# Performance work log

Measured on AMD Instinct MI355X. Metric: run time of the kernel, lower is better.

The kernel has to match this reference:

```python
import jax, jax.numpy as jnp
import numpy as np

D_MODEL = 1024
NUM_HEADS = 16
D_K = D_MODEL // NUM_HEADS


def setup_inputs() -> dict:
    key = jax.random.key(0)
    ks = jax.random.split(key, 11)
    B, S = 1, 4096
    s = 1.0 / np.sqrt(D_MODEL)
    return {
        "query": jax.random.normal(ks[0], (B, S, D_MODEL), jnp.float32),
        "key": jax.random.normal(ks[1], (B, S, D_MODEL), jnp.float32),
        "value": jax.random.normal(ks[2], (B, S, D_MODEL), jnp.float32),
        "Wq": jax.random.normal(ks[3], (D_MODEL, D_MODEL), jnp.float32) * s,
        "bq": jnp.zeros((D_MODEL,), jnp.float32),
        "Wk": jax.random.normal(ks[4], (D_MODEL, D_MODEL), jnp.float32) * s,
        "bk": jnp.zeros((D_MODEL,), jnp.float32),
        "Wv": jax.random.normal(ks[5], (D_MODEL, D_MODEL), jnp.float32) * s,
        "bv": jnp.zeros((D_MODEL,), jnp.float32),
        "Wo": jax.random.normal(ks[6], (D_MODEL, D_MODEL), jnp.float32) * s,
        "bo": jnp.zeros((D_MODEL,), jnp.float32),
    }


def reference(query, key, value, Wq, bq, Wk, bk, Wv, bv, Wo, bo):
    B, S, _ = query.shape
    # linear projections, split into heads: [B, H, S, d_k]
    def proj(x, W, b):
        y = x @ W.T + b
        return y.reshape(B, -1, NUM_HEADS, D_K).transpose(0, 2, 1, 3)

    q = proj(query, Wq, bq)
    k = proj(key, Wk, bk)
    v = proj(value, Wv, bv)

    scale = D_K ** (-0.5)
    scores = jnp.einsum("bhqd,bhkd->bhqk", q, k) * scale  # [B,H,S,S]
    attn = jax.nn.softmax(scores, axis=-1)
    out = jnp.einsum("bhqk,bhkd->bhqd", attn, v)  # [B,H,S,d_k]
    out = out.transpose(0, 2, 1, 3).reshape(B, -1, NUM_HEADS * D_K)
    return out @ Wo.T + bo
```

## Files before the change

### kernel.cpp

```cpp
#include <hip/hip_runtime.h>

typedef __bf16 bf16;
typedef __bf16 bf16x8 __attribute__((ext_vector_type(8)));
typedef __bf16 bf16x4 __attribute__((ext_vector_type(4)));
typedef float floatx4 __attribute__((ext_vector_type(4)));

#define MFMA(a, b, c) __builtin_amdgcn_mfma_f32_16x16x32_bf16((a), (b), (c), 0, 0, 0)

__device__ inline bf16x8 load8(const bf16* p) { return *(const bf16x8*)(p); }
__device__ inline bf16x4 load4(const bf16* p) { return *(const bf16x4*)(p); }
__device__ inline bf16x8 cat44(bf16x4 a, bf16x4 b) {
    return __builtin_shufflevector(a, b, 0, 1, 2, 3, 4, 5, 6, 7);
}

__device__ inline void store_c(bf16* p, float v) { *p = (bf16)v; }
__device__ inline void store_c(float* p, float v) { *p = v; }

__device__ inline float fast_exp2(float x) {
#if __has_builtin(__builtin_amdgcn_exp2f)
    return __builtin_amdgcn_exp2f(x);
#else
    float r;
    asm("v_exp_f32 %0, %1" : "=v"(r) : "v"(x));
    return r;
#endif
}

__device__ inline float fast_rcp(float x) {
#if __has_builtin(__builtin_amdgcn_rcpf)
    return __builtin_amdgcn_rcpf(x);
#else
    float r;
    asm("v_rcp_f32 %0, %1" : "=v"(r) : "v"(x));
    return r;
#endif
}

__device__ inline void gload_lds(const bf16* g, bf16* l) {
    __builtin_amdgcn_global_load_lds(
        (const __attribute__((address_space(1))) void*)(g),
        (__attribute__((address_space(3))) void*)(l), 16, 0, 0);
}

struct CvtArgs {
    const float* src[7];
    bf16* dst[7];
    int n[7];
};
__global__ __launch_bounds__(256) void cvt_bf16(CvtArgs a) {
    const int t = blockIdx.y;
    const int i = (blockIdx.x * 256 + threadIdx.x) * 8;
    if (i >= a.n[t]) return;
    const float4 u = *(const float4*)(a.src[t] + i);
    const float4 v = *(const float4*)(a.src[t] + i + 4);
    bf16x8 r;
    r[0] = (bf16)u.x; r[1] = (bf16)u.y; r[2] = (bf16)u.z; r[3] = (bf16)u.w;
    r[4] = (bf16)v.x; r[5] = (bf16)v.y; r[6] = (bf16)v.z; r[7] = (bf16)v.w;
    *(bf16x8*)(a.dst[t] + i) = r;
}

template <typename TC>
__device__ inline void gemm_core(const bf16* __restrict__ A, const bf16* __restrict__ W,
                                 const float* __restrict__ bias, TC* __restrict__ C,
                                 bool TR) {
    __shared__ bf16 As[2][128][32];
    __shared__ bf16 Bs[2][128][32];

    const int tid = threadIdx.x;
    const int wv = tid >> 6, lane = tid & 63;
    const int quad = lane >> 4, lo = lane & 15;
    const int wm = wv >> 1, wn = wv & 1;
    const int Ar0 = blockIdx.y * 128, Br0 = blockIdx.x * 128;

    const int srow = lane >> 2, sseg = (lane & 3) ^ (srow & 3);
    const bf16* Ag = A + (size_t)(Ar0 + srow) * 1024 + sseg * 8;
    const bf16* Bg = W + (size_t)(Br0 + srow) * 1024 + sseg * 8;

    auto stage = [&](int buf, int k0) {
#pragma unroll
        for (int c = 2 * wv; c < 2 * wv + 2; c++) {
            gload_lds(Ag + (size_t)c * 16 * 1024 + k0, &As[buf][c * 16][0]);
            gload_lds(Bg + (size_t)c * 16 * 1024 + k0, &Bs[buf][c * 16][0]);
        }
    };

    floatx4 acc[4][4] = {};
    const int rs = (quad ^ (lo & 3)) * 8;

    stage(0, 0);
    for (int k0 = 0; k0 < 1024; k0 += 32) {
        const int buf = (k0 >> 5) & 1;
        __syncthreads();
        if (k0 + 32 < 1024) stage(buf ^ 1, k0 + 32);

        bf16x8 a[4], b[4];
#pragma unroll
        for (int i = 0; i < 4; i++) a[i] = load8(&As[buf][wm * 64 + i * 16 + lo][rs]);
#pragma unroll
        for (int j = 0; j < 4; j++) b[j] = load8(&Bs[buf][wn * 64 + j * 16 + lo][rs]);
#pragma unroll
        for (int i = 0; i < 4; i++)
#pragma unroll
            for (int j = 0; j < 4; j++) acc[i][j] = MFMA(a[i], b[j], acc[i][j]);
    }

#pragma unroll
    for (int i = 0; i < 4; i++) {
#pragma unroll
        for (int j = 0; j < 4; j++) {
#pragma unroll
            for (int r = 0; r < 4; r++) {
                const int m = Ar0 + wm * 64 + i * 16 + quad * 4 + r;
                const int n = Br0 + wn * 64 + j * 16 + lo;
                const float v = acc[i][j][r] + bias[n];
                if (!TR) {
                    store_c(C + (size_t)m * 1024 + n, v);
                } else {
                    store_c(C + (size_t)(n >> 6) * (64 * 4096) + (size_t)(n & 63) * 4096 + m, v);
                }
            }
        }
    }
}

__global__ __launch_bounds__(256) void gemm_qkv(
    const bf16* __restrict__ qb, const bf16* __restrict__ kb, const bf16* __restrict__ vb,
    const bf16* __restrict__ Wq, const bf16* __restrict__ Wk, const bf16* __restrict__ Wv,
    const float* __restrict__ bq, const float* __restrict__ bk, const float* __restrict__ bv,
    bf16* __restrict__ Q, bf16* __restrict__ Kp, bf16* __restrict__ Vt) {
    if (blockIdx.z == 0)
        gemm_core<bf16>(qb, Wq, bq, Q, false);
    else if (blockIdx.z == 1)
        gemm_core<bf16>(kb, Wk, bk, Kp, false);
    else
        gemm_core<bf16>(vb, Wv, bv, Vt, true);
}

__global__ __launch_bounds__(256) void gemm_o(const bf16* __restrict__ O,
                                              const bf16* __restrict__ Wo,
                                              const float* __restrict__ bo,
                                              float* __restrict__ out) {
    gemm_core<float>(O, Wo, bo, out, false);
}

__global__ __launch_bounds__(512) void flash_attn14(const bf16* __restrict__ Q,
                                                    const bf16* __restrict__ Kmat,
                                                    const bf16* __restrict__ Vt,
                                                    float* __restrict__ Pp,
                                                    float* __restrict__ lb) {
    __shared__ bf16 Ks[4][64][64];
    __shared__ bf16 Vs[4][64][64];

    const int tid = threadIdx.x;
    const int wv = tid >> 6;
    const int lane = tid & 63;
    const int quad = lane >> 4, lo = lane & 15;
    const int h = blockIdx.x;
    const int qb = blockIdx.y;
    const int z = blockIdx.z;
    const int kv0 = z * 2048;
    const int DM = 1024;
    const int q0 = qb * 256 + wv * 32;

    float* myP = Pp + (size_t)z * 4096 * 1024;
    float* myl = lb + z * 65536 + h * 4096;

    bf16x8 aQ[2][2];
#pragma unroll
    for (int qs = 0; qs < 2; qs++) {
        const bf16* qp = Q + (size_t)(q0 + qs * 16 + lo) * DM + h * 64 + quad * 8;
        aQ[qs][0] = load8(qp);
        aQ[qs][1] = load8(qp + 32);
    }

    bf16x8 bOnes;
#pragma unroll
    for (int i = 0; i < 8; i++) bOnes[i] = (bf16)1.0f;

    floatx4 Oacc[2][4] = {};
    floatx4 Lacc[2] = {};

    const int srow = lane >> 3, sseg = (lane & 7) ^ srow;
    const bf16* Kg = Kmat + (size_t)srow * DM + h * 64 + sseg * 8;
    const bf16* Vg = Vt + (size_t)h * 64 * 4096 + (size_t)srow * 4096 + sseg * 8;

    auto stage = [&](int buf, int kb2) {
        gload_lds(Kg + (size_t)(kb2 + wv * 8) * DM, &Ks[buf][wv * 8][0]);
        gload_lds(Vg + (size_t)(wv * 8) * 4096 + kb2, &Vs[buf][wv * 8][0]);
    };

    const float C_SCALE = 0.18033688011112043f;
    const float C_BIAS = 23.083120654223415f;
    const int sw = lo & 7;
    const int vo = quad >> 1;
    const int vlo = (quad & 1) * 4;

    auto body = [&](int buf) {
        floatx4 st[2][4];
        __builtin_amdgcn_s_setprio(1);
#pragma unroll
        for (int t = 0; t < 4; t++) {
            const bf16* krow = &Ks[buf][t * 16 + lo][0];
            const bf16x8 aK0 = load8(krow + ((quad ^ sw) * 8));
            const bf16x8 aK1 = load8(krow + (((quad + 4) ^ sw) * 8));
#pragma unroll
            for (int qs = 0; qs < 2; qs++) {
                floatx4 zz = {};
                zz = MFMA(aK0, aQ[qs][0], zz);
                st[qs][t] = MFMA(aK1, aQ[qs][1], zz);
            }
        }
        __builtin_amdgcn_s_setprio(0);

        bf16x4 pp[2][4];
#pragma unroll
        for (int qs = 0; qs < 2; qs++)
#pragma unroll
            for (int t = 0; t < 4; t++)
#pragma unroll
                for (int r = 0; r < 4; r++)
                    pp[qs][t][r] = (bf16)fast_exp2(fmaf(st[qs][t][r], C_SCALE, -C_BIAS));

        __builtin_amdgcn_s_setprio(1);
#pragma unroll
        for (int kk = 0; kk < 2; kk++) {
            const bf16x8 aP0 = cat44(pp[0][2 * kk], pp[0][2 * kk + 1]);
            const bf16x8 aP1 = cat44(pp[1][2 * kk], pp[1][2 * kk + 1]);
            Lacc[0] = MFMA(aP0, bOnes, Lacc[0]);
            Lacc[1] = MFMA(aP1, bOnes, Lacc[1]);
#pragma unroll
            for (int nt = 0; nt < 4; nt++) {
                const bf16* vrow = &Vs[buf][nt * 16 + lo][0];
                const bf16x4 v0 = load4(vrow + (((kk * 4 + vo) ^ sw) << 3) + vlo);
                const bf16x4 v1 = load4(vrow + (((kk * 4 + 2 + vo) ^ sw) << 3) + vlo);
                const bf16x8 bV = cat44(v0, v1);
                Oacc[0][nt] = MFMA(aP0, bV, Oacc[0][nt]);
                Oacc[1][nt] = MFMA(aP1, bV, Oacc[1][nt]);
            }
        }
        __builtin_amdgcn_s_setprio(0);
    };

    stage(0, kv0);
    stage(1, kv0 + 64);
    for (int p = 0; p < 16; p++) {
        const int ba = (p & 1) * 2;
        __syncthreads();
        if (p + 1 < 16) {
            const int nk = kv0 + (p + 1) * 128;
            stage(ba ^ 2, nk);
            stage((ba ^ 2) + 1, nk + 64);
        }
        body(ba);
        body(ba + 1);
    }

#pragma unroll
    for (int qs = 0; qs < 2; qs++)
#pragma unroll
        for (int r = 0; r < 4; r++) {
            const int row = q0 + qs * 16 + quad * 4 + r;
            if (lo == 0) myl[row] = Lacc[qs][r];
#pragma unroll
            for (int nt = 0; nt < 4; nt++) {
                myP[(size_t)row * DM + h * 64 + nt * 16 + lo] = Oacc[qs][nt][r];
            }
        }
}

template <int NZ>
__global__ __launch_bounds__(256) void combine_n(const float* __restrict__ P,
                                                 const float* __restrict__ lb,
                                                 bf16* __restrict__ Ob) {
    const size_t i = (size_t)(blockIdx.x * 256 + threadIdx.x) * 8;
    const int row = (int)(i >> 10), col = (int)(i & 1023), h = col >> 6;
    float l = 0.f;
#pragma unroll
    for (int z = 0; z < NZ; z++) l += lb[z * 65536 + h * 4096 + row];
    const float inv = fast_rcp(l);
    float acc[8] = {};
#pragma unroll
    for (int z = 0; z < NZ; z++) {
        const float4 a0 = *(const float4*)(P + (size_t)z * 4194304 + i);
        const float4 a1 = *(const float4*)(P + (size_t)z * 4194304 + i + 4);
        acc[0] += a0.x; acc[1] += a0.y; acc[2] += a0.z; acc[3] += a0.w;
        acc[4] += a1.x; acc[5] += a1.y; acc[6] += a1.z; acc[7] += a1.w;
    }
    bf16x8 r;
#pragma unroll
    for (int j = 0; j < 8; j++) r[j] = (bf16)(acc[j] * inv);
    *(bf16x8*)(Ob + i) = r;
}

extern "C" void kernel_launch(void* const* d_in, const int* in_sizes, int n_in,
                              void* d_out, int out_size, void* d_ws, size_t ws_size,
                              hipStream_t stream) {
    const float* query = (const float*)d_in[0];
    const float* key_i = (const float*)d_in[1];
    const float* value = (const float*)d_in[2];
    const float* Wq = (const float*)d_in[3];
    const float* bq = (const float*)d_in[4];
    const float* Wk = (const float*)d_in[5];
    const float* bk = (const float*)d_in[6];
    const float* Wv = (const float*)d_in[7];
    const float* bv = (const float*)d_in[8];
    const float* Wo = (const float*)d_in[9];
    const float* bo = (const float*)d_in[10];

    bf16* ws = (bf16*)d_ws;
    const size_t SZ = (size_t)4096 * 1024;
    const size_t WZ = (size_t)1024 * 1024;
    const int SZi = 4096 * 1024, WZi = 1024 * 1024;
    bf16* qb = ws;
    bf16* kb = ws + SZ;
    bf16* vb = ws + 2 * SZ;
    bf16* Wqb = ws + 3 * SZ;
    bf16* Wkb = ws + 3 * SZ + WZ;
    bf16* Wvb = ws + 3 * SZ + 2 * WZ;
    bf16* Q = ws + 3 * SZ + 4 * WZ;
    bf16* K = Q + SZ;
    bf16* Vt = Q + 2 * SZ;
    bf16* Wob = ws + 6 * SZ + 4 * WZ;
    float* lbuf = (float*)(ws + 6 * SZ + 5 * WZ);
    float* Pp = (float*)ws;
    bf16* O = Q;

    CvtArgs ca;
    ca.src[0] = query; ca.dst[0] = qb;  ca.n[0] = SZi;
    ca.src[1] = key_i; ca.dst[1] = kb;  ca.n[1] = SZi;
    ca.src[2] = value; ca.dst[2] = vb;  ca.n[2] = SZi;
    ca.src[3] = Wq;    ca.dst[3] = Wqb; ca.n[3] = WZi;
    ca.src[4] = Wk;    ca.dst[4] = Wkb; ca.n[4] = WZi;
    ca.src[5] = Wv;    ca.dst[5] = Wvb; ca.n[5] = WZi;
    ca.src[6] = Wo;    ca.dst[6] = Wob; ca.n[6] = WZi;
    cvt_bf16<<<dim3(2048, 7), 256, 0, stream>>>(ca);

    gemm_qkv<<<dim3(8, 32, 3), 256, 0, stream>>>(qb, kb, vb, Wqb, Wkb, Wvb,
                                                 bq, bk, bv, Q, K, Vt);
    flash_attn14<<<dim3(16, 16, 2), 512, 0, stream>>>(Q, K, Vt, Pp, lbuf);
    combine_n<2><<<2048, 256, 0, stream>>>(Pp, lbuf, O);
    gemm_o<<<dim3(8, 32), 256, 0, stream>>>(O, Wob, bo, (float*)d_out);
}
```

Measured before the change: 261.8 us.

## Fold softmax scale into Q projection, permute V layout, narrow output GEMM tiles

Multiplies the Q projection output by the softmax log2 scale and seeds the score MFMA accumulator with the negative bias, removing the per-score FMA before exp2. V^T is written in a permuted column order so each lane reads its PV operand with one 8-element LDS load instead of two 4-element loads. The output projection uses 128x64 tiles to launch twice as many blocks. Scaling Q before bf16 rounding slightly changes numerics.

```diff
diff --git a/kernel.cpp b/kernel.cpp
--- a/kernel.cpp
+++ b/kernel.cpp
@@ -6,6 +6,8 @@
 typedef float floatx4 __attribute__((ext_vector_type(4)));
 
 #define MFMA(a, b, c) __builtin_amdgcn_mfma_f32_16x16x32_bf16((a), (b), (c), 0, 0, 0)
+
+#define QSCALE 0.18033688011112043f
 
 __device__ inline bf16x8 load8(const bf16* p) { return *(const bf16x8*)(p); }
 __device__ inline bf16x4 load4(const bf16* p) { return *(const bf16x4*)(p); }
@@ -62,7 +64,7 @@
 template <typename TC>
 __device__ inline void gemm_core(const bf16* __restrict__ A, const bf16* __restrict__ W,
                                  const float* __restrict__ bias, TC* __restrict__ C,
-                                 bool TR) {
+                                 bool TR, float oscale) {
     __shared__ bf16 As[2][128][32];
     __shared__ bf16 Bs[2][128][32];
 
@@ -112,11 +114,14 @@
             for (int r = 0; r < 4; r++) {
                 const int m = Ar0 + wm * 64 + i * 16 + quad * 4 + r;
                 const int n = Br0 + wn * 64 + j * 16 + lo;
-                const float v = acc[i][j][r] + bias[n];
+                const float v = (acc[i][j][r] + bias[n]) * oscale;
                 if (!TR) {
                     store_c(C + (size_t)m * 1024 + n, v);
                 } else {
-                    store_c(C + (size_t)(n >> 6) * (64 * 4096) + (size_t)(n & 63) * 4096 + m, v);
+                    const int p64 = (i >> 1) * 32 + quad * 8 + (i & 1) * 4 + r;
+                    store_c(C + (size_t)(n >> 6) * (64 * 4096) + (size_t)(n & 63) * 4096 +
+                                (Ar0 + wm * 64 + p64),
+                            v);
                 }
             }
         }
@@ -129,21 +134,70 @@
     const float* __restrict__ bq, const float* __restrict__ bk, const float* __restrict__ bv,
     bf16* __restrict__ Q, bf16* __restrict__ Kp, bf16* __restrict__ Vt) {
     if (blockIdx.z == 0)
-        gemm_core<bf16>(qb, Wq, bq, Q, false);
+        gemm_core<bf16>(qb, Wq, bq, Q, false, QSCALE);
     else if (blockIdx.z == 1)
-        gemm_core<bf16>(kb, Wk, bk, Kp, false);
+        gemm_core<bf16>(kb, Wk, bk, Kp, false, 1.0f);
     else
-        gemm_core<bf16>(vb, Wv, bv, Vt, true);
-}
-
-__global__ __launch_bounds__(256) void gemm_o(const bf16* __restrict__ O,
-                                              const bf16* __restrict__ Wo,
-                                              const float* __restrict__ bo,
-                                              float* __restrict__ out) {
-    gemm_core<float>(O, Wo, bo, out, false);
-}
-
-__global__ __launch_bounds__(512) void flash_attn14(const bf16* __restrict__ Q,
+        gemm_core<bf16>(vb, Wv, bv, Vt, true, 1.0f);
+}
+
+__global__ __launch_bounds__(256) void gemm_o64(const bf16* __restrict__ O,
+                                                const bf16* __restrict__ Wo,
+                                                const float* __restrict__ bo,
+                                                float* __restrict__ out) {
+    __shared__ bf16 As[2][128][32];
+    __shared__ bf16 Bs[2][64][32];
+
+    const int tid = threadIdx.x;
+    const int wv = tid >> 6, lane = tid & 63;
+    const int quad = lane >> 4, lo = lane & 15;
+    const int wm = wv >> 1, wn = wv & 1;
+    const int Ar0 = blockIdx.y * 128, Br0 = blockIdx.x * 64;
+
+    const int srow = lane >> 2, sseg = (lane & 3) ^ (srow & 3);
+    const bf16* Ag = O + (size_t)(Ar0 + srow) * 1024 + sseg * 8;
+    const bf16* Bg = Wo + (size_t)(Br0 + srow) * 1024 + sseg * 8;
+
+    auto stage = [&](int buf, int k0) {
+#pragma unroll
+        for (int c = 2 * wv; c < 2 * wv + 2; c++)
+            gload_lds(Ag + (size_t)c * 16 * 1024 + k0, &As[buf][c * 16][0]);
+        gload_lds(Bg + (size_t)wv * 16 * 1024 + k0, &Bs[buf][wv * 16][0]);
+    };
+
+    floatx4 acc[4][2] = {};
+    const int rs = (quad ^ (lo & 3)) * 8;
+
+    stage(0, 0);
+    for (int k0 = 0; k0 < 1024; k0 += 32) {
+        const int buf = (k0 >> 5) & 1;
+        __syncthreads();
+        if (k0 + 32 < 1024) stage(buf ^ 1, k0 + 32);
+
+        bf16x8 a[4], b[2];
+#pragma unroll
+        for (int i = 0; i < 4; i++) a[i] = load8(&As[buf][wm * 64 + i * 16 + lo][rs]);
+#pragma unroll
+        for (int j = 0; j < 2; j++) b[j] = load8(&Bs[buf][wn * 32 + j * 16 + lo][rs]);
+#pragma unroll
+        for (int i = 0; i < 4; i++)
+#pragma unroll
+            for (int j = 0; j < 2; j++) acc[i][j] = MFMA(a[i], b[j], acc[i][j]);
+    }
+
+#pragma unroll
+    for (int i = 0; i < 4; i++)
+#pragma unroll
+        for (int j = 0; j < 2; j++)
+#pragma unroll
+            for (int r = 0; r < 4; r++) {
+                const int m = Ar0 + wm * 64 + i * 16 + quad * 4 + r;
+                const int n = Br0 + wn * 32 + j * 16 + lo;
+                out[(size_t)m * 1024 + n] = acc[i][j][r] + bo[n];
+            }
+}
+
+__global__ __launch_bounds__(512) void flash_attn15(const bf16* __restrict__ Q,
                                                     const bf16* __restrict__ Kmat,
                                                     const bf16* __restrict__ Vt,
                                                     float* __restrict__ Pp,
@@ -180,6 +234,9 @@
     floatx4 Oacc[2][4] = {};
     floatx4 Lacc[2] = {};
 
+    const float C_BIAS = 23.083120654223415f;
+    const floatx4 zinit = {-C_BIAS, -C_BIAS, -C_BIAS, -C_BIAS};
+
     const int srow = lane >> 3, sseg = (lane & 7) ^ srow;
     const bf16* Kg = Kmat + (size_t)srow * DM + h * 64 + sseg * 8;
     const bf16* Vg = Vt + (size_t)h * 64 * 4096 + (size_t)srow * 4096 + sseg * 8;
@@ -189,11 +246,7 @@
         gload_lds(Vg + (size_t)(wv * 8) * 4096 + kb2, &Vs[buf][wv * 8][0]);
     };
 
-    const float C_SCALE = 0.18033688011112043f;
-    const float C_BIAS = 23.083120654223415f;
     const int sw = lo & 7;
-    const int vo = quad >> 1;
-    const int vlo = (quad & 1) * 4;
 
     auto body = [&](int buf) {
         floatx4 st[2][4];
@@ -205,8 +258,7 @@
             const bf16x8 aK1 = load8(krow + (((quad + 4) ^ sw) * 8));
 #pragma unroll
             for (int qs = 0; qs < 2; qs++) {
-                floatx4 zz = {};
-                zz = MFMA(aK0, aQ[qs][0], zz);
+                const floatx4 zz = MFMA(aK0, aQ[qs][0], zinit);
                 st[qs][t] = MFMA(aK1, aQ[qs][1], zz);
             }
         }
@@ -219,7 +271,7 @@
             for (int t = 0; t < 4; t++)
 #pragma unroll
                 for (int r = 0; r < 4; r++)
-                    pp[qs][t][r] = (bf16)fast_exp2(fmaf(st[qs][t][r], C_SCALE, -C_BIAS));
+                    pp[qs][t][r] = (bf16)fast_exp2(st[qs][t][r]);
 
         __builtin_amdgcn_s_setprio(1);
 #pragma unroll
@@ -230,10 +282,7 @@
             Lacc[1] = MFMA(aP1, bOnes, Lacc[1]);
 #pragma unroll
             for (int nt = 0; nt < 4; nt++) {
-                const bf16* vrow = &Vs[buf][nt * 16 + lo][0];
-                const bf16x4 v0 = load4(vrow + (((kk * 4 + vo) ^ sw) << 3) + vlo);
-                const bf16x4 v1 = load4(vrow + (((kk * 4 + 2 + vo) ^ sw) << 3) + vlo);
-                const bf16x8 bV = cat44(v0, v1);
+                const bf16x8 bV = load8(&Vs[buf][nt * 16 + lo][(((kk * 4 + quad) ^ sw) * 8)]);
                 Oacc[0][nt] = MFMA(aP0, bV, Oacc[0][nt]);
                 Oacc[1][nt] = MFMA(aP1, bV, Oacc[1][nt]);
             }
@@ -337,7 +386,7 @@
 
     gemm_qkv<<<dim3(8, 32, 3), 256, 0, stream>>>(qb, kb, vb, Wqb, Wkb, Wvb,
                                                  bq, bk, bv, Q, K, Vt);
-    flash_attn14<<<dim3(16, 16, 2), 512, 0, stream>>>(Q, K, Vt, Pp, lbuf);
+    flash_attn15<<<dim3(16, 16, 2), 512, 0, stream>>>(Q, K, Vt, Pp, lbuf);
     combine_n<2><<<2048, 256, 0, stream>>>(Pp, lbuf, O);
-    gemm_o<<<dim3(8, 32), 256, 0, stream>>>(O, Wob, bo, (float*)d_out);
-}
+    gemm_o64<<<dim3(16, 32), 256, 0, stream>>>(O, Wob, bo, (float*)d_out);
+}
```

Result: no change. 260.0 us (-0.7%).
